# Optimization experiments

Hardware: AMD Instinct MI355X
Metric: run time of the kernel (lower is better)

The kernel has to match this reference:

```python
import jax, jax.numpy as jnp
import numpy as np

B, C, H, W = 64, 256, 64, 64
HEADS = 8
Q = 16
FH = 512
EPS = 1e-6


def setup_inputs() -> dict:
    key = jax.random.key(0)
    ks = jax.random.split(key, 4)
    def init(k, shape, fan_in):
        return jax.random.normal(k, shape, jnp.float32) * (1.0 / np.sqrt(fan_in))
    return {
        "x": jax.random.normal(ks[0], (B, C, H, W), jnp.float32),
        "ln_gamma": jnp.ones((C,), jnp.float32),
        "ln_beta": jnp.zeros((C,), jnp.float32),
        # grouped 1x1 conv weight: torch shape [Q*h, C/h, 1, 1] -> [h, Q, C/h]
        "attn_w": init(ks[1], (HEADS, Q, C // HEADS), C // HEADS),
        "val_w": init(ks[2], (C, C), C),
        "val_b": jnp.zeros((C,), jnp.float32),
        "fin_w": init(ks[3], (FH, C * Q), C * Q),
        "fin_b": jnp.zeros((FH,), jnp.float32),
    }


def reference(x, ln_gamma, ln_beta, attn_w, val_w, val_b, fin_w, fin_b):
    B_, C_, H_, W_ = x.shape
    L = H_ * W_
    xf = x.reshape(B_, C_, L)  # [B, C, HW]
    # LayerNorm2d: normalize over channel dim (permute in torch == axis=1 here)
    mu = jnp.mean(xf, axis=1, keepdims=True)
    var = jnp.mean((xf - mu) ** 2, axis=1, keepdims=True)
    xn = (xf - mu) * jax.lax.rsqrt(var + EPS) * ln_gamma[:, None] + ln_beta[:, None]
    # grouped 1x1 conv: each head sees its own C/h channel slice
    xh = xn.reshape(B_, HEADS, C_ // HEADS, L)
    logits = jnp.einsum('hqc,bhcl->bhql', attn_w, xh)  # [B, h, Q, HW]
    Aw = jax.nn.softmax(logits, axis=-1)
    # value projection: full 1x1 conv with bias
    V = jnp.einsum('ec,bcl->bel', val_w, xn) + val_b[None, :, None]  # [B, C, HW]
    Vh = V.reshape(B_, HEADS, C_ // HEADS, L)
    # weighted pooling (bmm): [B, h, Q, d]
    A = jnp.einsum('bhql,bhdl->bhqd', Aw, Vh)
    Aflat = A.reshape(B_, Q * C_)  # matches torch reshape order (h, q, d)
    return Aflat @ fin_w.T + fin_b
```

## Files before the change

### kernel.cpp

```cpp
#include <hip/hip_runtime.h>

typedef unsigned short u16;
typedef unsigned int u32;

#define B_   64
#define C_   256
#define L_   4096
#define NH   8
#define NQ   16
#define DH   32
#define HQ   128
#define FHN  512
#define EPS_ 1e-6f

#define WS_WC    0
#define WS_SWG   8192
#define WS_CB    8704
#define WS_DENP  9216
#define WS_SNUP  271360
#define WS_A     533504
#define WS_PP    1582080

typedef __attribute__((ext_vector_type(8))) short bf16x8;
typedef __attribute__((ext_vector_type(4))) float f32x4;

__device__ __forceinline__ u16 f32_to_bf16(float f) {
    u32 u = __float_as_uint(f);
    u32 r = u + 0x7fffu + ((u >> 16) & 1u);
    return (u16)(r >> 16);
}
__device__ __forceinline__ float bf16_to_f32(u16 h) {
    return __uint_as_float(((u32)h) << 16);
}
__device__ __forceinline__ u32 pk2(u16 lo, u16 hi) {
    return (u32)lo | ((u32)hi << 16);
}

__global__ __launch_bounds__(256) void k_prep(
    const float* __restrict__ attn_w, const float* __restrict__ gamma,
    const float* __restrict__ beta, u16* __restrict__ wc,
    float* __restrict__ Swg, float* __restrict__ Cb)
{
    int t = threadIdx.x;
    if (t >= HQ) return;
    int h = t >> 4;
    float sw = 0.f, cb = 0.f;
    for (int c = 0; c < DH; c++) {
        float w = attn_w[t * DH + c];
        u16 hb = f32_to_bf16(w * gamma[h * DH + c]);
        wc[t * DH + c] = hb;
        sw += bf16_to_f32(hb);
        cb += w * beta[h * DH + c];
    }
    Swg[t] = sw;
    Cb[t] = cb;
}

__global__ __launch_bounds__(256) void k_fused(
    const float* __restrict__ x, const u16* __restrict__ wc,
    const float* __restrict__ Swg, const float* __restrict__ Cb,
    float* __restrict__ Pp, float* __restrict__ DenP, float* __restrict__ SnuP)
{
    __shared__ u16 XT[32 * 264];
    __shared__ u16 EA[128 * 40];
    __shared__ u16 XC[2][256 * 32];
    __shared__ float smu[32], srs[32];
    int t = threadIdx.x;
    int lane = t & 63, wv = t >> 6;
    int lane15 = lane & 15, quad = lane >> 4;
    int ks = blockIdx.x, b = blockIdx.y;
    int lbase = ks * 512;
    int m0 = (wv & 1) * 64, n0 = (wv >> 1) * 128;

    bf16x8 af[2];
    float swr[2][4], cbr[2][4];
    #pragma unroll
    for (int s = 0; s < 2; s++) {
        int h = wv * 2 + s;
        af[s] = *(const bf16x8*)(wc + (size_t)(h * 16 + lane15) * DH + quad * 8);
        #pragma unroll
        for (int r = 0; r < 4; r++) {
            int hq = h * 16 + quad * 4 + r;
            swr[s][r] = Swg[hq];
            cbr[s][r] = Cb[hq];
        }
    }

    const float* xR = x + ((size_t)b * C_ + t) * L_ + lbase;

    float4 fr[8];
    uint4 pr[4];
    auto loadregs = [&](int k) {
        int o = k * 32;
        #pragma unroll
        for (int i = 0; i < 8; i++) fr[i] = *(const float4*)(xR + o + i * 4);
    };
    auto cvtregs = [&]() {
        const float* pf = (const float*)fr;
        u16 hh[32];
        #pragma unroll
        for (int e = 0; e < 32; e++) hh[e] = f32_to_bf16(pf[e]);
        #pragma unroll
        for (int i = 0; i < 4; i++) {
            uint4 w;
            w.x = pk2(hh[i * 8 + 0], hh[i * 8 + 1]);
            w.y = pk2(hh[i * 8 + 2], hh[i * 8 + 3]);
            w.z = pk2(hh[i * 8 + 4], hh[i * 8 + 5]);
            w.w = pk2(hh[i * 8 + 6], hh[i * 8 + 7]);
            pr[i] = w;
        }
    };
    auto write_xc = [&](int buf) {
        #pragma unroll
        for (int i = 0; i < 4; i++)
            *(uint4*)&XC[buf][t * 32 + ((i ^ (t & 3)) * 8)] = pr[i];
    };
    auto write_xt = [&]() {
        const u16* ph = (const u16*)pr;
        #pragma unroll
        for (int e = 0; e < 32; e++) XT[e * 264 + t] = ph[e];
    };

    f32x4 acc[4][8];
    #pragma unroll
    for (int i = 0; i < 4; i++)
        #pragma unroll
        for (int j = 0; j < 8; j++) {
            f32x4 z = {0.f, 0.f, 0.f, 0.f};
            acc[i][j] = z;
        }
    float se[2][4] = {}, sm[2][4] = {};

    int l_loc = t >> 3, g = t & 7;

    loadregs(0);
    cvtregs();
    write_xt();
    write_xc(0);
    loadregs(1);
    __syncthreads();

    for (int k = 0; k < 16; k++) {
        int cur = k & 1;

        {
            const u16* row = XT + l_loc * 264 + g * 32;
            float s = 0.f, q = 0.f;
            #pragma unroll
            for (int j = 0; j < 4; j++) {
                uint4 v = *(const uint4*)(row + j * 8);
                u32 ww[4] = {v.x, v.y, v.z, v.w};
                #pragma unroll
                for (int e = 0; e < 4; e++) {
                    float f0 = __uint_as_float(ww[e] << 16);
                    float f1 = __uint_as_float(ww[e] & 0xffff0000u);
                    s += f0 + f1;
                    q += f0 * f0 + f1 * f1;
                }
            }
            #pragma unroll
            for (int off = 1; off < 8; off <<= 1) {
                s += __shfl_xor(s, off);
                q += __shfl_xor(q, off);
            }
            if (g == 0) {
                float mm = s * (1.f / C_);
                float vv = fmaxf(q * (1.f / C_) - mm * mm, 0.f) + EPS_;
                smu[l_loc] = mm;
                srs[l_loc] = rsqrtf(vv);
            }
        }
        __syncthreads();

        #pragma unroll
        for (int half = 0; half < 2; half++) {
            float m_l = smu[half * 16 + lane15];
            float r_l = srs[half * 16 + lane15];
            #pragma unroll
            for (int s = 0; s < 2; s++) {
                int h = wv * 2 + s;
                bf16x8 bfrag = *(const bf16x8*)(XT + (half * 16 + lane15) * 264 + h * DH + quad * 8);
                f32x4 z = {0.f, 0.f, 0.f, 0.f};
                f32x4 c4 = __builtin_amdgcn_mfma_f32_16x16x32_bf16(af[s], bfrag, z, 0, 0, 0);
                #pragma unroll
                for (int r = 0; r < 4; r++) {
                    float logit = r_l * (c4[r] - m_l * swr[s][r]) + cbr[s][r];
                    float e = __expf(logit);
                    float ers = e * r_l;
                    EA[(h * 16 + quad * 4 + r) * 40 + half * 16 + lane15] = f32_to_bf16(ers);
                    se[s][r] += e;
                    sm[s][r] += ers * m_l;
                }
            }
        }
        __syncthreads();

        if (k < 15) { cvtregs(); write_xt(); write_xc(cur ^ 1); }
        if (k < 14) loadregs(k + 2);

        bf16x8 a[4];
        #pragma unroll
        for (int i = 0; i < 4; i++)
            a[i] = *(const bf16x8*)&EA[(m0 + i * 16 + lane15) * 40 + quad * 8];
        #pragma unroll
        for (int j = 0; j < 8; j++) {
            int row = n0 + j * 16 + lane15;
            bf16x8 bbj = *(const bf16x8*)&XC[cur][row * 32 + ((quad ^ (row & 3)) * 8)];
            #pragma unroll
            for (int i = 0; i < 4; i++)
                acc[i][j] = __builtin_amdgcn_mfma_f32_16x16x32_bf16(a[i], bbj, acc[i][j], 0, 0, 0);
        }
        __syncthreads();
    }

    float* PpB = Pp + (((size_t)ks * B_ + b) * HQ) * C_;
    #pragma unroll
    for (int i = 0; i < 4; i++)
        #pragma unroll
        for (int r = 0; r < 4; r++) {
            int hq = m0 + i * 16 + quad * 4 + r;
            #pragma unroll
            for (int j = 0; j < 8; j++)
                PpB[(size_t)hq * C_ + n0 + j * 16 + lane15] = acc[i][j][r];
        }

    #pragma unroll
    for (int s = 0; s < 2; s++)
        #pragma unroll
        for (int r = 0; r < 4; r++) {
            float v = se[s][r], w = sm[s][r];
            #pragma unroll
            for (int off = 1; off < 16; off <<= 1) {
                v += __shfl_xor(v, off);
                w += __shfl_xor(w, off);
            }
            if (lane15 == 0) {
                int row = b * HQ + (wv * 2 + s) * 16 + quad * 4 + r;
                DenP[ks * (B_ * HQ) + row] = v;
                SnuP[ks * (B_ * HQ) + row] = w;
            }
        }
}

__global__ __launch_bounds__(256) void k_attn_pool(
    const float* __restrict__ Pp, const float* __restrict__ DenP,
    const float* __restrict__ SnuP, const float* __restrict__ gamma,
    const float* __restrict__ beta, const float* __restrict__ val_w,
    const float* __restrict__ val_b, float* __restrict__ A)
{
    __shared__ float Pt[NQ * 257];
    __shared__ float Vw[DH * 257];
    __shared__ float vb_s[DH];
    int t = threadIdx.x;
    int h = blockIdx.x, b = blockIdx.y;

    for (int i = t; i < DH * C_; i += 256) {
        int r = i >> 8, c = i & 255;
        Vw[r * 257 + c] = val_w[(h * DH + r) * C_ + c];
    }
    if (t < DH) vb_s[t] = val_b[h * DH + t];

    const float* PpB = Pp + ((size_t)b * HQ + h * NQ) * C_;
    const size_t sstr = (size_t)B_ * HQ * C_;
    for (int i = t; i < NQ * C_; i += 256) {
        int q = i >> 8, c = i & 255;
        int row = b * HQ + h * NQ + q;
        float d = 0.f, sn = 0.f;
        #pragma unroll
        for (int s = 0; s < 8; s++) {
            d += DenP[s * (B_ * HQ) + row];
            sn += SnuP[s * (B_ * HQ) + row];
        }
        float pv = 0.f;
        #pragma unroll
        for (int s = 0; s < 8; s++) pv += PpB[s * sstr + (size_t)q * C_ + c];
        Pt[q * 257 + c] = gamma[c] * (pv - sn) / d + beta[c];
    }
    __syncthreads();

    int q = t >> 4, dd = (t & 15) * 2;
    float a0 = vb_s[dd], a1 = vb_s[dd + 1];
    for (int c = 0; c < C_; c++) {
        float pv = Pt[q * 257 + c];
        a0 += pv * Vw[dd * 257 + c];
        a1 += pv * Vw[(dd + 1) * 257 + c];
    }
    size_t off = ((size_t)(b * HQ + h * NQ + q)) * DH + dd;
    A[off] = a0; A[off + 1] = a1;
}

__global__ __launch_bounds__(256) void k_final(
    const float* __restrict__ A, const float* __restrict__ fin_w,
    const float* __restrict__ fin_b, float* __restrict__ out)
{
    __shared__ float At[64 * 129];
    __shared__ float Fw[32 * 129];
    int t = threadIdx.x;
    int kc = blockIdx.x, ft = blockIdx.y;
    int k0 = kc * 128;

    #pragma unroll
    for (int w = 0; w < 8; w++) {
        int s = t + w * 256;
        int row = s >> 5, seg = s & 31;
        float4 v = *(const float4*)(A + (size_t)row * 4096 + k0 + seg * 4);
        const float* pf = (const float*)&v;
        #pragma unroll
        for (int e = 0; e < 4; e++) At[row * 129 + seg * 4 + e] = pf[e];
    }
    #pragma unroll
    for (int w = 0; w < 4; w++) {
        int s = t + w * 256;
        int row = s >> 5, seg = s & 31;
        float4 v = *(const float4*)(fin_w + (size_t)(ft * 32 + row) * 4096 + k0 + seg * 4);
        const float* pf = (const float*)&v;
        #pragma unroll
        for (int e = 0; e < 4; e++) Fw[row * 129 + seg * 4 + e] = pf[e];
    }
    __syncthreads();

    int tb = t >> 3, tf = t & 7;
    float acc[2][4];
    #pragma unroll
    for (int e = 0; e < 2; e++)
        #pragma unroll
        for (int j = 0; j < 4; j++) acc[e][j] = 0.f;

    for (int k = 0; k < 128; k++) {
        float a0 = At[(tb * 2) * 129 + k];
        float a1 = At[(tb * 2 + 1) * 129 + k];
        #pragma unroll
        for (int j = 0; j < 4; j++) {
            float f = Fw[(tf * 4 + j) * 129 + k];
            acc[0][j] += a0 * f;
            acc[1][j] += a1 * f;
        }
    }
    #pragma unroll
    for (int e = 0; e < 2; e++) {
        int brow = tb * 2 + e;
        #pragma unroll
        for (int j = 0; j < 4; j++) {
            int f = ft * 32 + tf * 4 + j;
            float v = acc[e][j];
            if (kc == 0) v += fin_b[f];
            atomicAdd(&out[(size_t)brow * FHN + f], v);
        }
    }
}

extern "C" void kernel_launch(void* const* d_in, const int* in_sizes, int n_in,
                              void* d_out, int out_size, void* d_ws, size_t ws_size,
                              hipStream_t stream) {
    const float* x      = (const float*)d_in[0];
    const float* gamma  = (const float*)d_in[1];
    const float* beta   = (const float*)d_in[2];
    const float* attn_w = (const float*)d_in[3];
    const float* val_w  = (const float*)d_in[4];
    const float* val_b  = (const float*)d_in[5];
    const float* fin_w  = (const float*)d_in[6];
    const float* fin_b  = (const float*)d_in[7];
    float* out = (float*)d_out;
    char* ws = (char*)d_ws;

    u16*   wc    = (u16*)(ws + WS_WC);
    float* Swg   = (float*)(ws + WS_SWG);
    float* Cb    = (float*)(ws + WS_CB);
    float* DenP  = (float*)(ws + WS_DENP);
    float* SnuP  = (float*)(ws + WS_SNUP);
    float* A     = (float*)(ws + WS_A);
    float* Pp    = (float*)(ws + WS_PP);

    hipMemsetAsync(out, 0, (size_t)B_ * FHN * sizeof(float), stream);

    k_prep<<<dim3(1), dim3(256), 0, stream>>>(attn_w, gamma, beta, wc, Swg, Cb);
    k_fused<<<dim3(8, 64), dim3(256), 0, stream>>>(x, wc, Swg, Cb, Pp, DenP, SnuP);
    k_attn_pool<<<dim3(8, 64), dim3(256), 0, stream>>>(Pp, DenP, SnuP, gamma,
                                                       beta, val_w, val_b, A);
    k_final<<<dim3(32, 16), dim3(256), 0, stream>>>(A, fin_w, fin_b, out);
}
```

Before: 442.4 us.

## Fold value projection into fused kernel epilogue to shrink split-K partials

Folds the LayerNorm gamma into the value weights (precomputed as bf16, together with per-row gamma and beta sums) and applies the per-head value projection inside the fused kernel's epilogue with MFMA. Each split-K block now writes partials of size 128x32 instead of 128x256, and the attention-pool kernel becomes a light reduce kernel. This is meant to remove most of the partial-sum write and read-back traffic and the scalar FP32 projection. In exchange the pooled tile is rounded to bf16 before the projection, which adds rounding error, and it adds an extra small prep launch.

```diff
diff --git a/kernel.cpp b/kernel.cpp
--- a/kernel.cpp
+++ b/kernel.cpp
@@ -16,10 +16,13 @@
 #define WS_WC    0
 #define WS_SWG   8192
 #define WS_CB    8704
-#define WS_DENP  9216
-#define WS_SNUP  271360
-#define WS_A     533504
-#define WS_PP    1582080
+#define WS_VGC   9216
+#define WS_WG1   140288
+#define WS_WB1   141312
+#define WS_DENP  142336
+#define WS_SNUP  404480
+#define WS_A     666624
+#define WS_APART 1715200
 
 typedef __attribute__((ext_vector_type(8))) short bf16x8;
 typedef __attribute__((ext_vector_type(4))) float f32x4;
@@ -56,14 +59,45 @@
     Cb[t] = cb;
 }
 
+__global__ __launch_bounds__(256) void k_prepv(
+    const float* __restrict__ val_w, const float* __restrict__ gamma,
+    const float* __restrict__ beta, u16* __restrict__ VGc,
+    float* __restrict__ Wg1, float* __restrict__ Wb1)
+{
+    int t = threadIdx.x;
+    int e = blockIdx.x * 4 + (t >> 6);
+    int lane = t & 63;
+    float4 w  = *(const float4*)(val_w + (size_t)e * C_ + lane * 4);
+    float4 g  = *(const float4*)(gamma + lane * 4);
+    float4 bt = *(const float4*)(beta + lane * 4);
+    u16 h0 = f32_to_bf16(w.x * g.x);
+    u16 h1 = f32_to_bf16(w.y * g.y);
+    u16 h2 = f32_to_bf16(w.z * g.z);
+    u16 h3 = f32_to_bf16(w.w * g.w);
+    uint2 pk;
+    pk.x = pk2(h0, h1);
+    pk.y = pk2(h2, h3);
+    *(uint2*)(VGc + (size_t)e * C_ + lane * 4) = pk;
+    float sg = bf16_to_f32(h0) + bf16_to_f32(h1) + bf16_to_f32(h2) + bf16_to_f32(h3);
+    float sb = w.x * bt.x + w.y * bt.y + w.z * bt.z + w.w * bt.w;
+    #pragma unroll
+    for (int off = 1; off < 64; off <<= 1) {
+        sg += __shfl_xor(sg, off);
+        sb += __shfl_xor(sb, off);
+    }
+    if (lane == 0) { Wg1[e] = sg; Wb1[e] = sb; }
+}
+
 __global__ __launch_bounds__(256) void k_fused(
     const float* __restrict__ x, const u16* __restrict__ wc,
     const float* __restrict__ Swg, const float* __restrict__ Cb,
-    float* __restrict__ Pp, float* __restrict__ DenP, float* __restrict__ SnuP)
+    const u16* __restrict__ VGc, float* __restrict__ Apart,
+    float* __restrict__ DenP, float* __restrict__ SnuP)
 {
-    __shared__ u16 XT[32 * 264];
-    __shared__ u16 EA[128 * 40];
-    __shared__ u16 XC[2][256 * 32];
+    __shared__ __align__(16) char POOL[67584];
+    u16* const XT  = (u16*)POOL;
+    u16* const EA  = (u16*)(POOL + 16896);
+    u16* const XCb = (u16*)(POOL + 27136);
     __shared__ float smu[32], srs[32];
     int t = threadIdx.x;
     int lane = t & 63, wv = t >> 6;
@@ -113,7 +147,7 @@
     auto write_xc = [&](int buf) {
         #pragma unroll
         for (int i = 0; i < 4; i++)
-            *(uint4*)&XC[buf][t * 32 + ((i ^ (t & 3)) * 8)] = pr[i];
+            *(uint4*)&XCb[buf * 8192 + t * 32 + ((i ^ (t & 3)) * 8)] = pr[i];
     };
     auto write_xt = [&]() {
         const u16* ph = (const u16*)pr;
@@ -205,7 +239,7 @@
         #pragma unroll
         for (int j = 0; j < 8; j++) {
             int row = n0 + j * 16 + lane15;
-            bf16x8 bbj = *(const bf16x8*)&XC[cur][row * 32 + ((quad ^ (row & 3)) * 8)];
+            bf16x8 bbj = *(const bf16x8*)&XCb[cur * 8192 + row * 32 + ((quad ^ (row & 3)) * 8)];
             #pragma unroll
             for (int i = 0; i < 4; i++)
                 acc[i][j] = __builtin_amdgcn_mfma_f32_16x16x32_bf16(a[i], bbj, acc[i][j], 0, 0, 0);
@@ -213,16 +247,37 @@
         __syncthreads();
     }
 
-    float* PpB = Pp + (((size_t)ks * B_ + b) * HQ) * C_;
+    u16* const P = (u16*)POOL;
     #pragma unroll
     for (int i = 0; i < 4; i++)
         #pragma unroll
-        for (int r = 0; r < 4; r++) {
-            int hq = m0 + i * 16 + quad * 4 + r;
-            #pragma unroll
-            for (int j = 0; j < 8; j++)
-                PpB[(size_t)hq * C_ + n0 + j * 16 + lane15] = acc[i][j][r];
-        }
+        for (int j = 0; j < 8; j++) {
+            int row = m0 + i * 16 + quad * 4;
+            int col = n0 + j * 16 + lane15;
+            #pragma unroll
+            for (int r = 0; r < 4; r++)
+                P[(row + r) * 264 + col] = f32_to_bf16(acc[i][j][r]);
+        }
+    __syncthreads();
+
+    float* ApB = Apart + (((size_t)ks * B_ + b) * HQ) * DH;
+    #pragma unroll
+    for (int s = 0; s < 2; s++) {
+        int h = wv * 2 + s;
+        #pragma unroll
+        for (int dt = 0; dt < 2; dt++) {
+            f32x4 c2 = {0.f, 0.f, 0.f, 0.f};
+            #pragma unroll
+            for (int kk = 0; kk < 8; kk++) {
+                bf16x8 a = *(const bf16x8*)&P[(h * 16 + lane15) * 264 + kk * 32 + quad * 8];
+                bf16x8 vg = *(const bf16x8*)(VGc + (size_t)(h * DH + dt * 16 + lane15) * C_ + kk * 32 + quad * 8);
+                c2 = __builtin_amdgcn_mfma_f32_16x16x32_bf16(a, vg, c2, 0, 0, 0);
+            }
+            #pragma unroll
+            for (int r = 0; r < 4; r++)
+                ApB[(size_t)(h * 16 + quad * 4 + r) * DH + dt * 16 + lane15] = c2[r];
+        }
+    }
 
     #pragma unroll
     for (int s = 0; s < 2; s++)
@@ -242,51 +297,41 @@
         }
 }
 
-__global__ __launch_bounds__(256) void k_attn_pool(
-    const float* __restrict__ Pp, const float* __restrict__ DenP,
-    const float* __restrict__ SnuP, const float* __restrict__ gamma,
-    const float* __restrict__ beta, const float* __restrict__ val_w,
-    const float* __restrict__ val_b, float* __restrict__ A)
+__global__ __launch_bounds__(256) void k_reduce(
+    const float* __restrict__ Apart, const float* __restrict__ DenP,
+    const float* __restrict__ SnuP, const float* __restrict__ Wg1,
+    const float* __restrict__ Wb1, const float* __restrict__ val_b,
+    float* __restrict__ A)
 {
-    __shared__ float Pt[NQ * 257];
-    __shared__ float Vw[DH * 257];
-    __shared__ float vb_s[DH];
+    __shared__ float sden[32], ssnu[32];
     int t = threadIdx.x;
-    int h = blockIdx.x, b = blockIdx.y;
-
-    for (int i = t; i < DH * C_; i += 256) {
-        int r = i >> 8, c = i & 255;
-        Vw[r * 257 + c] = val_w[(h * DH + r) * C_ + c];
-    }
-    if (t < DH) vb_s[t] = val_b[h * DH + t];
-
-    const float* PpB = Pp + ((size_t)b * HQ + h * NQ) * C_;
-    const size_t sstr = (size_t)B_ * HQ * C_;
-    for (int i = t; i < NQ * C_; i += 256) {
-        int q = i >> 8, c = i & 255;
-        int row = b * HQ + h * NQ + q;
+    int q4 = blockIdx.x, b = blockIdx.y;
+    int hq0 = q4 * 32;
+    if (t < 32) {
+        int row = b * HQ + hq0 + t;
         float d = 0.f, sn = 0.f;
         #pragma unroll
         for (int s = 0; s < 8; s++) {
-            d += DenP[s * (B_ * HQ) + row];
+            d  += DenP[s * (B_ * HQ) + row];
             sn += SnuP[s * (B_ * HQ) + row];
         }
-        float pv = 0.f;
-        #pragma unroll
-        for (int s = 0; s < 8; s++) pv += PpB[s * sstr + (size_t)q * C_ + c];
-        Pt[q * 257 + c] = gamma[c] * (pv - sn) / d + beta[c];
+        sden[t] = d;
+        ssnu[t] = sn;
     }
     __syncthreads();
-
-    int q = t >> 4, dd = (t & 15) * 2;
-    float a0 = vb_s[dd], a1 = vb_s[dd + 1];
-    for (int c = 0; c < C_; c++) {
-        float pv = Pt[q * 257 + c];
-        a0 += pv * Vw[dd * 257 + c];
-        a1 += pv * Vw[(dd + 1) * 257 + c];
-    }
-    size_t off = ((size_t)(b * HQ + h * NQ + q)) * DH + dd;
-    A[off] = a0; A[off + 1] = a1;
+    #pragma unroll
+    for (int i = 0; i < 4; i++) {
+        int idx = i * 256 + t;
+        int r32 = idx >> 5, d = idx & 31;
+        int hq = hq0 + r32;
+        float v = 0.f;
+        #pragma unroll
+        for (int s = 0; s < 8; s++)
+            v += Apart[(((size_t)s * B_ + b) * HQ + hq) * DH + d];
+        int hd = (hq >> 4) * DH + d;
+        A[((size_t)b * HQ + hq) * DH + d] =
+            (v - ssnu[r32] * Wg1[hd]) / sden[r32] + Wb1[hd] + val_b[hd];
+    }
 }
 
 __global__ __launch_bounds__(256) void k_final(
@@ -366,16 +411,21 @@
     u16*   wc    = (u16*)(ws + WS_WC);
     float* Swg   = (float*)(ws + WS_SWG);
     float* Cb    = (float*)(ws + WS_CB);
+    u16*   VGc   = (u16*)(ws + WS_VGC);
+    float* Wg1   = (float*)(ws + WS_WG1);
+    float* Wb1   = (float*)(ws + WS_WB1);
     float* DenP  = (float*)(ws + WS_DENP);
     float* SnuP  = (float*)(ws + WS_SNUP);
     float* A     = (float*)(ws + WS_A);
-    float* Pp    = (float*)(ws + WS_PP);
+    float* Apart = (float*)(ws + WS_APART);
 
     hipMemsetAsync(out, 0, (size_t)B_ * FHN * sizeof(float), stream);
 
     k_prep<<<dim3(1), dim3(256), 0, stream>>>(attn_w, gamma, beta, wc, Swg, Cb);
-    k_fused<<<dim3(8, 64), dim3(256), 0, stream>>>(x, wc, Swg, Cb, Pp, DenP, SnuP);
-    k_attn_pool<<<dim3(8, 64), dim3(256), 0, stream>>>(Pp, DenP, SnuP, gamma,
-                                                       beta, val_w, val_b, A);
+    k_prepv<<<dim3(64), dim3(256), 0, stream>>>(val_w, gamma, beta, VGc, Wg1, Wb1);
+    k_fused<<<dim3(8, 64), dim3(256), 0, stream>>>(x, wc, Swg, Cb, VGc, Apart,
+                                                   DenP, SnuP);
+    k_reduce<<<dim3(4, 64), dim3(256), 0, stream>>>(Apart, DenP, SnuP, Wg1, Wb1,
+                                                    val_b, A);
     k_final<<<dim3(32, 16), dim3(256), 0, stream>>>(A, fin_w, fin_b, out);
 }
```

Result: faster. 431.0 us (-2.6%).
